# Kernel tuning notes

Measured on AMD Instinct MI355X. Metric: run time of the kernel, lower is better.

Reference implementation:

```python
import jax, jax.numpy as jnp
import numpy as np

N_LAYERS = 6
D_MODEL = 256
D_STATE_C = 32  # d_state=64 real -> 32 complex conjugate pairs
N_MELS = 128
NUM_CLASSES = 50
BATCH = 16
SEQ = 2048


def setup_inputs() -> dict:
    key = jax.random.key(0)
    ks = jax.random.split(key, 16)
    H, N, NL = D_MODEL, D_STATE_C, N_LAYERS
    dt_min, dt_max = 1e-3, 1e-1
    log_dt = (jax.random.uniform(ks[0], (NL, H)) * (np.log(dt_max) - np.log(dt_min))
              + np.log(dt_min)).astype(jnp.float32)
    # S4D-Lin style init for the diagonal state matrix (proxy for NPLR legs)
    A_re = -0.5 * jnp.ones((NL, H, N), jnp.float32)
    A_im = jnp.broadcast_to(np.pi * jnp.arange(N, dtype=jnp.float32), (NL, H, N))
    A_im = jnp.asarray(A_im)
    return {
        'x': jax.random.normal(ks[1], (BATCH, SEQ, N_MELS), jnp.float32),
        'W_in': jax.random.normal(ks[2], (N_MELS, H), jnp.float32) / np.sqrt(N_MELS),
        'b_in': jnp.zeros((H,), jnp.float32),
        'log_dt': log_dt,
        'A_re': A_re,
        'A_im': A_im,
        'B_re': jax.random.normal(ks[3], (NL, H, N), jnp.float32),
        'B_im': jax.random.normal(ks[4], (NL, H, N), jnp.float32),
        'C_re': jax.random.normal(ks[5], (NL, H, N), jnp.float32),
        'C_im': jax.random.normal(ks[6], (NL, H, N), jnp.float32),
        'D': jax.random.normal(ks[7], (NL, H), jnp.float32),
        'W_out': jax.random.normal(ks[8], (NL, H, 2 * H), jnp.float32) / np.sqrt(H),
        'b_out': jnp.zeros((NL, 2 * H), jnp.float32),
        'ln_scale': jnp.ones((NL, H), jnp.float32),
        'ln_bias': jnp.zeros((NL, H), jnp.float32),
        'ln_f_scale': jnp.ones((H,), jnp.float32),
        'ln_f_bias': jnp.zeros((H,), jnp.float32),
        'W_cls': jax.random.normal(ks[9], (H, NUM_CLASSES), jnp.float32) / np.sqrt(H),
        'b_cls': jnp.zeros((NUM_CLASSES,), jnp.float32),
    }


def _layer_norm(x, scale, bias, eps=1e-5):
    mu = jnp.mean(x, axis=-1, keepdims=True)
    var = jnp.mean(jnp.square(x - mu), axis=-1, keepdims=True)
    return (x - mu) * jax.lax.rsqrt(var + eps) * scale + bias


def _forward(x, W_in, b_in, log_dt, A_re, A_im, B_re, B_im, C_re, C_im, D,
             W_out, b_out, ln_scale, ln_bias, ln_f_scale, ln_f_bias, W_cls, b_cls):
    x = x @ W_in + b_in  # [B, L, H]
    L = x.shape[1]
    t = jnp.arange(L, dtype=jnp.float32)
    n_fft = 2 * L
    for i in range(N_LAYERS):
        z = _layer_norm(x, ln_scale[i], ln_bias[i])  # prenorm
        A = A_re[i] + 1j * A_im[i]                   # [H, N] complex diag
        Bc = B_re[i] + 1j * B_im[i]
        Cc = C_re[i] + 1j * C_im[i]
        dt = jnp.exp(log_dt[i])[:, None]             # [H, 1]
        dtA = dt * A
        dB = Bc * (jnp.exp(dtA) - 1.0) / A           # ZOH discretization
        # K[h, l] = 2 Re( sum_n C*dB * exp(l * dt * A) )  -- conjugate-pair SSM kernel
        van = jnp.exp(dtA[:, :, None] * t)            # [H, N, L]
        K = 2.0 * jnp.einsum('hn,hnl->hl', Cc * dB, van).real
        # FFT convolution along time
        u_f = jnp.fft.rfft(z, n=n_fft, axis=1)        # [B, n/2+1, H]
        k_f = jnp.fft.rfft(K, n=n_fft, axis=-1)       # [H, n/2+1]
        y = jnp.fft.irfft(u_f * k_f.T[None], n=n_fft, axis=1)[:, :L]
        y = y + z * D[i]                              # skip (D) term
        y = jax.nn.gelu(y)                            # activation
        v = y @ W_out[i] + b_out[i]                   # [B, L, 2H]
        a, g = jnp.split(v, 2, axis=-1)
        y = a * jax.nn.sigmoid(g)                     # GLU postact
        x = x + y                                     # residual 'R'
    x = _layer_norm(x, ln_f_scale, ln_f_bias)         # final prenorm norm
    pooled = jnp.mean(x, axis=1)                      # NDDecoder mode='pool'
    return pooled @ W_cls + b_cls                     # [B, num_classes]


def reference(x, W_in, b_in, log_dt, A_re, A_im, B_re, B_im, C_re, C_im, D,
              W_out, b_out, ln_scale, ln_bias, ln_f_scale, ln_f_bias, W_cls, b_cls):
    return _forward(x, W_in, b_in, log_dt, A_re, A_im, B_re, B_im, C_re, C_im, D,
                    W_out, b_out, ln_scale, ln_bias, ln_f_scale, ln_f_bias, W_cls, b_cls)
```

## Files before the change

### kernel.cpp

```cpp
#include <hip/hip_runtime.h>
#include <math.h>

#define NLAYERS 6
#define HD 256
#define NS 32
#define NCLS 50
#define BB 16
#define LL 2048
#define TT 64
#define CC 32

typedef __attribute__((ext_vector_type(8))) short bf16x8;
typedef __attribute__((ext_vector_type(4))) float f32x4;

__device__ __attribute__((aligned(16))) float g_x [8388608];
__device__ __attribute__((aligned(16))) float g_Vt[6389760];
__device__ __attribute__((aligned(16))) float g_Kt[98304];
__device__ __attribute__((aligned(16))) float g_E0[98304];
__device__ __attribute__((aligned(16))) float g_pp[65536];
__device__ __attribute__((aligned(16))) unsigned short g_zbh[8388608];
__device__ __attribute__((aligned(16))) unsigned short g_Mt [12582912];
__device__ __attribute__((aligned(16))) unsigned short g_TAt[6291456];
__device__ __attribute__((aligned(16))) unsigned short g_ybh[8388608];
__device__ __attribute__((aligned(16))) unsigned short g_yt [8388608];
__device__ __attribute__((aligned(16))) unsigned short g_Wt [786432];
__device__ __attribute__((aligned(16))) unsigned short g_xb [4194304];
__device__ __attribute__((aligned(16))) unsigned short g_Wint[32768];

__device__ __forceinline__ float sigf(float x) { return 1.0f / (1.0f + __expf(-x)); }
__device__ __forceinline__ float geluf(float x) {
  float t = 0.7978845608028654f * (x + 0.044715f * x * x * x);
  float e = __expf(2.0f * t);
  float th = 1.0f - 2.0f / (e + 1.0f);
  return 0.5f * x * (1.0f + th);
}
__device__ __forceinline__ unsigned short f2bf(float f) {
  unsigned u = __float_as_uint(f);
  unsigned r = (u + 0x7FFFu + ((u >> 16) & 1u)) >> 16;
  return (unsigned short)r;
}

__global__ void k_precomp(const float* __restrict__ log_dt,
                          const float* __restrict__ A_re, const float* __restrict__ A_im,
                          const float* __restrict__ B_re, const float* __restrict__ B_im,
                          const float* __restrict__ C_re, const float* __restrict__ C_im) {
  int id = blockIdx.x * 256 + threadIdx.x;
  if (id >= NLAYERS * HD * NS) return;
  int h = (id / NS) % HD;
  int i = id / (NS * HD);
  float dt = expf(log_dt[i * HD + h]);
  float ar = A_re[id], ai = A_im[id];
  float dr = dt * ar, di = dt * ai;
  float er = expf(dr);
  float wr = er * cosf(di), wi = er * sinf(di);
  float inv = 1.0f / (ar * ar + ai * ai);
  float mr = wr - 1.0f, mi = wi;
  float qr = (mr * ar + mi * ai) * inv;
  float qi = (mi * ar - mr * ai) * inv;
  float br = B_re[id], bi = B_im[id];
  float dbr = br * qr - bi * qi, dbi = br * qi + bi * qr;
  float cr = C_re[id], ci = C_im[id];
  g_E0[id * 2 + 0] = cr * dbr - ci * dbi;
  g_E0[id * 2 + 1] = cr * dbi + ci * dbr;
  float pr = 1.0f, pi = 0.0f;
  long base = (long)id * 65;
  for (int t = 0; t <= 64; ++t) {
    g_Vt[(base + t) * 2 + 0] = pr;
    g_Vt[(base + t) * 2 + 1] = pi;
    float nr = pr * wr - pi * wi;
    pi = pr * wi + pi * wr;
    pr = nr;
  }
}

__global__ void k_precompK() {
  int id = blockIdx.x * 256 + threadIdx.x;
  if (id >= NLAYERS * HD * TT) return;
  int t = id % TT;
  int lh = id / TT;
  float acc = 0.f;
  const float* e = g_E0 + (long)lh * NS * 2;
  const float* v = g_Vt + ((long)lh * NS * 65 + t) * 2;
  for (int n = 0; n < NS; ++n)
    acc += e[n * 2] * v[n * 130] - e[n * 2 + 1] * v[n * 130 + 1];
  g_Kt[id] = 2.0f * acc;
}

__global__ void k_precompM(const float* __restrict__ Dd) {
  int id = blockIdx.x * 256 + threadIdx.x;
  int k = id & 127;
  int t = (id >> 7) & 63;
  int lh = id >> 13;
  float v;
  if (k < 64) {
    v = (t >= k) ? g_Kt[(long)lh * 64 + (t - k)] : 0.f;
    if (k == t) v += Dd[lh];
  } else {
    int p = k - 64, n = p >> 1;
    const float2 w = ((const float2*)g_Vt)[((long)lh * NS + n) * 65 + (t + 1)];
    v = (p & 1) ? (-2.f * w.y) : (2.f * w.x);
  }
  g_Mt[id] = f2bf(v);
}

__global__ void k_precompA2() {
  int id = blockIdx.x * 256 + threadIdx.x;
  int t = id & 63;
  int p = (id >> 6) & 63;
  int lh = id >> 12;
  int n = p >> 1;
  const float2 w = ((const float2*)g_Vt)[((long)lh * NS + n) * 65 + (63 - t)];
  g_TAt[id] = f2bf((p & 1) ? w.y : w.x);
}

__global__ __launch_bounds__(256) void k_prepW(const float* __restrict__ W_out) {
  __shared__ float T[32][33];
  int bid = blockIdx.x;
  int nt = bid & 15, kt = (bid >> 4) & 7, l = bid >> 7;
  int t = threadIdx.x;
  int tr = t >> 3, tc = t & 7;
  const float* src = W_out + (long)l * 131072 + (long)(kt * 32) * 512 + nt * 32;
  float4 v = *(const float4*)(src + (long)tr * 512 + tc * 4);
  T[tr][tc * 4 + 0] = v.x; T[tr][tc * 4 + 1] = v.y;
  T[tr][tc * 4 + 2] = v.z; T[tr][tc * 4 + 3] = v.w;
  __syncthreads();
  ushort4 o;
  o.x = f2bf(T[tc * 4 + 0][tr]); o.y = f2bf(T[tc * 4 + 1][tr]);
  o.z = f2bf(T[tc * 4 + 2][tr]); o.w = f2bf(T[tc * 4 + 3][tr]);
  *(ushort4*)(g_Wt + ((long)l * 512 + nt * 32 + tr) * 256 + kt * 32 + tc * 4) = o;
}

__global__ void k_prepWin(const float* __restrict__ W_in) {
  int k = blockIdx.x, n = threadIdx.x;
  g_Wint[n * 128 + k] = f2bf(W_in[k * 256 + n]);
}

__global__ void k_castin(const float* __restrict__ xin) {
  long base = ((long)blockIdx.x * 256 + threadIdx.x) * 8;
  float4 v0 = *(const float4*)(xin + base);
  float4 v1 = *(const float4*)(xin + base + 4);
  union { unsigned short u[8]; ulonglong2 v; } pk;
  pk.u[0] = f2bf(v0.x); pk.u[1] = f2bf(v0.y); pk.u[2] = f2bf(v0.z); pk.u[3] = f2bf(v0.w);
  pk.u[4] = f2bf(v1.x); pk.u[5] = f2bf(v1.y); pk.u[6] = f2bf(v1.z); pk.u[7] = f2bf(v1.w);
  *(ulonglong2*)(g_xb + base) = pk.v;
}

__global__ __launch_bounds__(256) void k_gemmin(const float* __restrict__ bias) {
  __shared__ __attribute__((aligned(16))) unsigned short As[128 * 32];
  __shared__ __attribute__((aligned(16))) unsigned short Bs[256 * 32];
  const int tid = threadIdx.x;
  const int wave = tid >> 6, lane = tid & 63;
  const int m0 = blockIdx.x * 128;
  const int wm = wave & 1, wn = wave >> 1;
  const int n15 = lane & 15, kg = lane >> 4, q2 = kg * 8;
  f32x4 acc[4][8];
  #pragma unroll
  for (int a = 0; a < 4; ++a)
    #pragma unroll
    for (int b2 = 0; b2 < 8; ++b2) acc[a][b2] = (f32x4){0.f, 0.f, 0.f, 0.f};
  for (int k0 = 0; k0 < 128; k0 += 32) {
    __syncthreads();
    #pragma unroll
    for (int it = 0; it < 2; ++it) {
      int slot = it * 256 + wave * 64 + lane;
      int m = slot >> 2, ko = (slot & 3) * 8;
      __builtin_amdgcn_global_load_lds(
        (const __attribute__((address_space(1))) unsigned int*)(g_xb + (long)(m0 + m) * 128 + k0 + ko),
        (__attribute__((address_space(3))) unsigned int*)(As + (it * 256 + wave * 64) * 8),
        16, 0, 0);
    }
    #pragma unroll
    for (int it = 0; it < 4; ++it) {
      int slot = it * 256 + wave * 64 + lane;
      int n = slot >> 2, ko = (slot & 3) * 8;
      __builtin_amdgcn_global_load_lds(
        (const __attribute__((address_space(1))) unsigned int*)(g_Wint + (long)n * 128 + k0 + ko),
        (__attribute__((address_space(3))) unsigned int*)(Bs + (it * 256 + wave * 64) * 8),
        16, 0, 0);
    }
    __syncthreads();
    bf16x8 af[4], bn[8];
    #pragma unroll
    for (int mt = 0; mt < 4; ++mt)
      af[mt] = *(const bf16x8*)&As[(wm * 64 + mt * 16 + n15) * 32 + q2];
    #pragma unroll
    for (int j = 0; j < 8; ++j)
      bn[j] = *(const bf16x8*)&Bs[(wn * 128 + j * 16 + n15) * 32 + q2];
    #pragma unroll
    for (int mt = 0; mt < 4; ++mt)
      #pragma unroll
      for (int j = 0; j < 8; ++j)
        acc[mt][j] = __builtin_amdgcn_mfma_f32_16x16x32_bf16(af[mt], bn[j], acc[mt][j], 0, 0, 0);
  }
  #pragma unroll
  for (int j = 0; j < 8; ++j) {
    int col = wn * 128 + j * 16 + n15;
    float bb = bias[col];
    #pragma unroll
    for (int mt = 0; mt < 4; ++mt)
      #pragma unroll
      for (int r = 0; r < 4; ++r) {
        int row = m0 + wm * 64 + mt * 16 + kg * 4 + r;
        g_x[(long)row * 256 + col] = acc[mt][j][r] + bb;
      }
  }
}

__global__ __launch_bounds__(256) void k_ln(const float* __restrict__ gam,
                                            const float* __restrict__ bet) {
  __shared__ unsigned short S[32 * 264];
  const int bid = blockIdx.x;
  const int b = bid >> 6, l0 = (bid & 63) << 5;
  const int tid = threadIdx.x, w = tid >> 6, lane = tid & 63;
  float4 gv = *(const float4*)(gam + lane * 4);
  float4 bv = *(const float4*)(bet + lane * 4);
  for (int r = 0; r < 8; ++r) {
    int ll = w * 8 + r;
    float4 v = *(const float4*)(g_x + ((long)(b * LL + l0 + ll)) * HD + lane * 4);
    float s1 = v.x + v.y + v.z + v.w;
    float s2 = v.x * v.x + v.y * v.y + v.z * v.z + v.w * v.w;
    #pragma unroll
    for (int off = 32; off; off >>= 1) { s1 += __shfl_xor(s1, off); s2 += __shfl_xor(s2, off); }
    float mu = s1 * (1.0f / HD);
    float rs = rsqrtf(s2 * (1.0f / HD) - mu * mu + 1e-5f);
    ushort4 o;
    o.x = f2bf((v.x - mu) * rs * gv.x + bv.x);
    o.y = f2bf((v.y - mu) * rs * gv.y + bv.y);
    o.z = f2bf((v.z - mu) * rs * gv.z + bv.z);
    o.w = f2bf((v.w - mu) * rs * gv.w + bv.w);
    *(ushort4*)&S[ll * 264 + lane * 4] = o;
  }
  __syncthreads();
  unsigned short* zp = g_zbh + ((long)(b * HD + tid)) * LL + l0;
  #pragma unroll
  for (int seg = 0; seg < 4; ++seg) {
    union { unsigned short u[8]; ulonglong2 v; } pk;
    #pragma unroll
    for (int i = 0; i < 8; ++i) pk.u[i] = S[(seg * 8 + i) * 264 + tid];
    *(ulonglong2*)(zp + seg * 8) = pk.v;
  }
}

__global__ __launch_bounds__(256) void k_ssm(int layer) {
  __shared__ __attribute__((aligned(16))) unsigned short Zs[32 * 72];
  __shared__ __attribute__((aligned(16))) unsigned short Ts[64 * 72];
  __shared__ __attribute__((aligned(16))) unsigned short Ms[64 * 136];
  __shared__ float Ss[32 * 68];
  __shared__ __attribute__((aligned(16))) unsigned short Gs[32 * 72];
  const int tid = threadIdx.x, wave = tid >> 6, lane = tid & 63;
  const int h = blockIdx.x >> 4, b = blockIdx.x & 15;
  const long lh = (long)layer * HD + h;
  {
    int c = tid >> 3, off = (tid & 7) * 8;
    *(ulonglong2*)&Zs[c * 72 + off] =
        *(const ulonglong2*)(g_zbh + ((long)(b * HD + h)) * LL + c * 64 + off);
  }
  const unsigned short* Tg = g_TAt + lh * 4096;
  #pragma unroll
  for (int i = 0; i < 2; ++i) {
    int seg = tid + i * 256;
    int row = seg >> 3, sc = (seg & 7) * 8;
    *(ulonglong2*)&Ts[row * 72 + sc] = *(const ulonglong2*)(Tg + row * 64 + sc);
  }
  const unsigned short* Mg = g_Mt + lh * 8192;
  #pragma unroll
  for (int i = 0; i < 4; ++i) {
    int seg = tid + i * 256;
    int row = seg >> 4, sc = (seg & 15) * 8;
    *(ulonglong2*)&Ms[row * 136 + sc] = *(const ulonglong2*)(Mg + row * 128 + sc);
  }
  __syncthreads();
  const int n15 = lane & 15, kg = lane >> 4;
  const int mt = wave & 1;
  const int jb = (wave >> 1) * 2;
  const int c = mt * 16 + n15;
  {
    bf16x8 a0 = *(const bf16x8*)&Zs[c * 72 + kg * 8];
    bf16x8 a1 = *(const bf16x8*)&Zs[c * 72 + 32 + kg * 8];
    #pragma unroll
    for (int jj = 0; jj < 2; ++jj) {
      int j = jb + jj;
      bf16x8 b0 = *(const bf16x8*)&Ts[(j * 16 + n15) * 72 + kg * 8];
      bf16x8 b1 = *(const bf16x8*)&Ts[(j * 16 + n15) * 72 + 32 + kg * 8];
      f32x4 acc = (f32x4){0.f, 0.f, 0.f, 0.f};
      acc = __builtin_amdgcn_mfma_f32_16x16x32_bf16(a0, b0, acc, 0, 0, 0);
      acc = __builtin_amdgcn_mfma_f32_16x16x32_bf16(a1, b1, acc, 0, 0, 0);
      #pragma unroll
      for (int r = 0; r < 4; ++r)
        Ss[(mt * 16 + kg * 4 + r) * 68 + j * 16 + n15] = acc[r];
    }
  }
  __syncthreads();
  if (wave == 0 && lane < 32) {
    int n = lane;
    long vb = (lh * NS + n) * 65;
    float wtr = g_Vt[vb * 2 + 128], wti = g_Vt[vb * 2 + 129];
    float e0r = g_E0[(lh * NS + n) * 2], e0i = g_E0[(lh * NS + n) * 2 + 1];
    float sr = 0.f, si = 0.f;
    for (int cc = 0; cc < CC; ++cc) {
      float er = Ss[cc * 68 + 2 * n], ei = Ss[cc * 68 + 2 * n + 1];
      Gs[cc * 72 + 2 * n]     = f2bf(e0r * sr - e0i * si);
      Gs[cc * 72 + 2 * n + 1] = f2bf(e0r * si + e0i * sr);
      float nr = er + wtr * sr - wti * si;
      si      = ei + wtr * si + wti * sr;
      sr = nr;
    }
  }
  __syncthreads();
  {
    bf16x8 a0 = *(const bf16x8*)&Zs[c * 72 + kg * 8];
    bf16x8 a1 = *(const bf16x8*)&Zs[c * 72 + 32 + kg * 8];
    bf16x8 a2 = *(const bf16x8*)&Gs[c * 72 + kg * 8];
    bf16x8 a3 = *(const bf16x8*)&Gs[c * 72 + 32 + kg * 8];
    unsigned short* yrow = g_ybh + ((long)(b * HD + h)) * LL;
    #pragma unroll
    for (int jj = 0; jj < 2; ++jj) {
      int j = jb + jj;
      const unsigned short* mrow = &Ms[(j * 16 + n15) * 136];
      bf16x8 b0 = *(const bf16x8*)&mrow[kg * 8];
      bf16x8 b1 = *(const bf16x8*)&mrow[32 + kg * 8];
      bf16x8 b2 = *(const bf16x8*)&mrow[64 + kg * 8];
      bf16x8 b3 = *(const bf16x8*)&mrow[96 + kg * 8];
      f32x4 acc = (f32x4){0.f, 0.f, 0.f, 0.f};
      acc = __builtin_amdgcn_mfma_f32_16x16x32_bf16(a0, b0, acc, 0, 0, 0);
      acc = __builtin_amdgcn_mfma_f32_16x16x32_bf16(a1, b1, acc, 0, 0, 0);
      acc = __builtin_amdgcn_mfma_f32_16x16x32_bf16(a2, b2, acc, 0, 0, 0);
      acc = __builtin_amdgcn_mfma_f32_16x16x32_bf16(a3, b3, acc, 0, 0, 0);
      #pragma unroll
      for (int r = 0; r < 4; ++r)
        yrow[(mt * 16 + kg * 4 + r) * 64 + j * 16 + n15] = f2bf(geluf(acc[r]));
    }
  }
}

__global__ __launch_bounds__(256) void k_transp() {
  __shared__ unsigned short T[64][65];
  int bid = blockIdx.x;
  int ht = bid & 3, lt = (bid >> 2) & 31, b = bid >> 7;
  int t = threadIdx.x;
  int r = t >> 4, c = t & 15;
  #pragma unroll
  for (int i = 0; i < 4; ++i) {
    int hh = r + i * 16;
    ushort4 v = *(const ushort4*)(g_ybh + ((long)(b * 256 + ht * 64 + hh)) * 2048 + lt * 64 + c * 4);
    T[hh][c * 4 + 0] = v.x; T[hh][c * 4 + 1] = v.y;
    T[hh][c * 4 + 2] = v.z; T[hh][c * 4 + 3] = v.w;
  }
  __syncthreads();
  #pragma unroll
  for (int i = 0; i < 4; ++i) {
    int ll = r + i * 16;
    ushort4 o;
    o.x = T[c * 4 + 0][ll]; o.y = T[c * 4 + 1][ll];
    o.z = T[c * 4 + 2][ll]; o.w = T[c * 4 + 3][ll];
    *(ushort4*)(g_yt + ((long)(b * 2048 + lt * 64 + ll)) * 256 + ht * 64 + c * 4) = o;
  }
}

__global__ __launch_bounds__(256, 4) void k_gemmglu(int layer, const float* __restrict__ bias) {
  __shared__ __attribute__((aligned(16))) unsigned short As[64 * 32];
  __shared__ __attribute__((aligned(16))) unsigned short Bs[256 * 32];
  const int tid = threadIdx.x;
  const int wave = tid >> 6, lane = tid & 63;
  const int m0 = blockIdx.x * 64;
  const int gg = blockIdx.y;
  const int wm = wave & 1, wn = wave >> 1;
  const int n15 = lane & 15, kg = lane >> 4, q2 = kg * 8;
  const unsigned short* Ag = g_yt + (long)m0 * 256;
  const unsigned short* Wt = g_Wt + (long)layer * 131072;
  f32x4 acc[2][8];
  #pragma unroll
  for (int a = 0; a < 2; ++a)
    #pragma unroll
    for (int b2 = 0; b2 < 8; ++b2) acc[a][b2] = (f32x4){0.f, 0.f, 0.f, 0.f};
  for (int k0 = 0; k0 < 256; k0 += 32) {
    __syncthreads();
    {
      int slot = wave * 64 + lane;
      int m = slot >> 2, ko = (slot & 3) * 8;
      __builtin_amdgcn_global_load_lds(
        (const __attribute__((address_space(1))) unsigned int*)(Ag + (long)m * 256 + k0 + ko),
        (__attribute__((address_space(3))) unsigned int*)(As + (wave * 64) * 8),
        16, 0, 0);
    }
    #pragma unroll
    for (int it = 0; it < 4; ++it) {
      int slot = it * 256 + wave * 64 + lane;
      int np = slot >> 2, ko = (slot & 3) * 8;
      int n = gg * 128 + (np < 128 ? np : np + 128);
      __builtin_amdgcn_global_load_lds(
        (const __attribute__((address_space(1))) unsigned int*)(Wt + (long)n * 256 + k0 + ko),
        (__attribute__((address_space(3))) unsigned int*)(Bs + (it * 256 + wave * 64) * 8),
        16, 0, 0);
    }
    __syncthreads();
    bf16x8 af0 = *(const bf16x8*)&As[(wm * 32 + n15) * 32 + q2];
    bf16x8 af1 = *(const bf16x8*)&As[(wm * 32 + 16 + n15) * 32 + q2];
    #pragma unroll
    for (int j = 0; j < 4; ++j) {
      bf16x8 ba = *(const bf16x8*)&Bs[(wn * 64 + j * 16 + n15) * 32 + q2];
      acc[0][j] = __builtin_amdgcn_mfma_f32_16x16x32_bf16(af0, ba, acc[0][j], 0, 0, 0);
      acc[1][j] = __builtin_amdgcn_mfma_f32_16x16x32_bf16(af1, ba, acc[1][j], 0, 0, 0);
      bf16x8 bg = *(const bf16x8*)&Bs[(128 + wn * 64 + j * 16 + n15) * 32 + q2];
      acc[0][4 + j] = __builtin_amdgcn_mfma_f32_16x16x32_bf16(af0, bg, acc[0][4 + j], 0, 0, 0);
      acc[1][4 + j] = __builtin_amdgcn_mfma_f32_16x16x32_bf16(af1, bg, acc[1][4 + j], 0, 0, 0);
    }
  }
  #pragma unroll
  for (int j = 0; j < 4; ++j) {
    int col = gg * 128 + wn * 64 + j * 16 + n15;
    float ba = bias[col], bg = bias[col + 256];
    #pragma unroll
    for (int mt = 0; mt < 2; ++mt) {
      #pragma unroll
      for (int r = 0; r < 4; ++r) {
        int row = m0 + wm * 32 + mt * 16 + kg * 4 + r;
        float a = acc[mt][j][r] + ba;
        float g = acc[mt][4 + j][r] + bg;
        float* xp = g_x + (long)row * 256 + col;
        *xp += a * sigf(g);
      }
    }
  }
}

__global__ __launch_bounds__(256) void k_lnpool(const float* __restrict__ gam,
                                                const float* __restrict__ bet) {
  __shared__ float red[4][256];
  const int bid = blockIdx.x;
  const int b = bid >> 4, s = bid & 15;
  const int tid = threadIdx.x, w = tid >> 6, lane = tid & 63;
  float4 gv = *(const float4*)(gam + lane * 4);
  float4 bv = *(const float4*)(bet + lane * 4);
  float a0 = 0, a1 = 0, a2 = 0, a3 = 0;
  for (int r = 0; r < 32; ++r) {
    int l = s * 128 + w * 32 + r;
    float4 v = *(const float4*)(g_x + ((long)b * LL + l) * HD + lane * 4);
    float s1 = v.x + v.y + v.z + v.w;
    float s2 = v.x * v.x + v.y * v.y + v.z * v.z + v.w * v.w;
    #pragma unroll
    for (int off = 32; off; off >>= 1) { s1 += __shfl_xor(s1, off); s2 += __shfl_xor(s2, off); }
    float mu = s1 * (1.0f / HD);
    float rs = rsqrtf(s2 * (1.0f / HD) - mu * mu + 1e-5f);
    a0 += (v.x - mu) * rs * gv.x + bv.x;
    a1 += (v.y - mu) * rs * gv.y + bv.y;
    a2 += (v.z - mu) * rs * gv.z + bv.z;
    a3 += (v.w - mu) * rs * gv.w + bv.w;
  }
  red[w][lane * 4 + 0] = a0; red[w][lane * 4 + 1] = a1;
  red[w][lane * 4 + 2] = a2; red[w][lane * 4 + 3] = a3;
  __syncthreads();
  g_pp[(long)bid * HD + tid] = red[0][tid] + red[1][tid] + red[2][tid] + red[3][tid];
}

__global__ __launch_bounds__(256) void k_cls(const float* __restrict__ Wc,
                                             const float* __restrict__ bc,
                                             float* __restrict__ out) {
  __shared__ float pl[256];
  const int b = blockIdx.x, tid = threadIdx.x;
  float p = 0.f;
  #pragma unroll
  for (int s = 0; s < 16; ++s) p += g_pp[((long)b * 16 + s) * HD + tid];
  pl[tid] = p * (1.0f / LL);
  __syncthreads();
  if (tid < NCLS) {
    float acc = bc[tid];
    for (int h = 0; h < HD; ++h) acc += pl[h] * Wc[h * NCLS + tid];
    out[b * NCLS + tid] = acc;
  }
}

extern "C" void kernel_launch(void* const* d_in, const int* in_sizes, int n_in,
                              void* d_out, int out_size, void* d_ws, size_t ws_size,
                              hipStream_t stream) {
  (void)in_sizes; (void)n_in; (void)d_ws; (void)ws_size; (void)out_size;
  const float* x_in   = (const float*)d_in[0];
  const float* W_in   = (const float*)d_in[1];
  const float* b_in   = (const float*)d_in[2];
  const float* log_dt = (const float*)d_in[3];
  const float* A_re   = (const float*)d_in[4];
  const float* A_im   = (const float*)d_in[5];
  const float* B_re   = (const float*)d_in[6];
  const float* B_im   = (const float*)d_in[7];
  const float* C_re   = (const float*)d_in[8];
  const float* C_im   = (const float*)d_in[9];
  const float* Dd     = (const float*)d_in[10];
  const float* W_out  = (const float*)d_in[11];
  const float* b_out  = (const float*)d_in[12];
  const float* ln_s   = (const float*)d_in[13];
  const float* ln_b   = (const float*)d_in[14];
  const float* lnf_s  = (const float*)d_in[15];
  const float* lnf_b  = (const float*)d_in[16];
  const float* W_cls  = (const float*)d_in[17];
  const float* b_cl   = (const float*)d_in[18];
  float* out = (float*)d_out;

  k_precomp<<<192, 256, 0, stream>>>(log_dt, A_re, A_im, B_re, B_im, C_re, C_im);
  k_precompK<<<384, 256, 0, stream>>>();
  k_precompM<<<49152, 256, 0, stream>>>(Dd);
  k_precompA2<<<24576, 256, 0, stream>>>();
  k_prepW<<<768, 256, 0, stream>>>(W_out);
  k_prepWin<<<128, 256, 0, stream>>>(W_in);
  k_castin<<<2048, 256, 0, stream>>>(x_in);
  k_gemmin<<<256, 256, 0, stream>>>(b_in);
  for (int i = 0; i < NLAYERS; ++i) {
    k_ln<<<1024, 256, 0, stream>>>(ln_s + i * HD, ln_b + i * HD);
    k_ssm<<<4096, 256, 0, stream>>>(i);
    k_transp<<<2048, 256, 0, stream>>>();
    k_gemmglu<<<dim3(512, 2), 256, 0, stream>>>(i, b_out + i * 2 * HD);
  }
  k_lnpool<<<256, 256, 0, stream>>>(lnf_s, lnf_b);
  k_cls<<<16, 256, 0, stream>>>(W_cls, b_cl, out);
}
```

Before: 720.1 us.

## Fuse transpose and next-layer LayerNorm into GLU GEMM epilogue

Removes the separate transpose kernel by having the GLU GEMM read the SSM output in [B,H,L] layout directly and transpose it into shared memory. It also fuses the next layer's LayerNorm into the GEMM epilogue: each block now covers all 512 output columns for 32 rows, so it can compute row statistics and write normalized bf16 z in [B,H,L] layout. This cuts two kernel launches per layer and the associated global round trips of the activations. In exchange the blocks are smaller in M, the shared-memory footprint is larger, and the A-tile loads are narrow strided 8-byte reads.

After: 710.4 us. About the same (-1.3%).

```diff
diff --git a/kernel.cpp b/kernel.cpp
--- a/kernel.cpp
+++ b/kernel.cpp
@@ -22,7 +22,6 @@
 __device__ __attribute__((aligned(16))) unsigned short g_Mt [12582912];
 __device__ __attribute__((aligned(16))) unsigned short g_TAt[6291456];
 __device__ __attribute__((aligned(16))) unsigned short g_ybh[8388608];
-__device__ __attribute__((aligned(16))) unsigned short g_yt [8388608];
 __device__ __attribute__((aligned(16))) unsigned short g_Wt [786432];
 __device__ __attribute__((aligned(16))) unsigned short g_xb [4194304];
 __device__ __attribute__((aligned(16))) unsigned short g_Wint[32768];
@@ -333,41 +332,22 @@
   }
 }
 
-__global__ __launch_bounds__(256) void k_transp() {
-  __shared__ unsigned short T[64][65];
-  int bid = blockIdx.x;
-  int ht = bid & 3, lt = (bid >> 2) & 31, b = bid >> 7;
-  int t = threadIdx.x;
-  int r = t >> 4, c = t & 15;
-  #pragma unroll
-  for (int i = 0; i < 4; ++i) {
-    int hh = r + i * 16;
-    ushort4 v = *(const ushort4*)(g_ybh + ((long)(b * 256 + ht * 64 + hh)) * 2048 + lt * 64 + c * 4);
-    T[hh][c * 4 + 0] = v.x; T[hh][c * 4 + 1] = v.y;
-    T[hh][c * 4 + 2] = v.z; T[hh][c * 4 + 3] = v.w;
-  }
-  __syncthreads();
-  #pragma unroll
-  for (int i = 0; i < 4; ++i) {
-    int ll = r + i * 16;
-    ushort4 o;
-    o.x = T[c * 4 + 0][ll]; o.y = T[c * 4 + 1][ll];
-    o.z = T[c * 4 + 2][ll]; o.w = T[c * 4 + 3][ll];
-    *(ushort4*)(g_yt + ((long)(b * 2048 + lt * 64 + ll)) * 256 + ht * 64 + c * 4) = o;
-  }
-}
-
-__global__ __launch_bounds__(256, 4) void k_gemmglu(int layer, const float* __restrict__ bias) {
-  __shared__ __attribute__((aligned(16))) unsigned short As[64 * 32];
-  __shared__ __attribute__((aligned(16))) unsigned short Bs[256 * 32];
-  const int tid = threadIdx.x;
-  const int wave = tid >> 6, lane = tid & 63;
-  const int m0 = blockIdx.x * 64;
-  const int gg = blockIdx.y;
-  const int wm = wave & 1, wn = wave >> 1;
+__global__ __launch_bounds__(256, 4) void k_gemmglu(int layer, const float* __restrict__ bias,
+                                                    const float* __restrict__ gam,
+                                                    const float* __restrict__ bet,
+                                                    int writez) {
+  __shared__ __attribute__((aligned(16))) unsigned short As[32 * 40];
+  __shared__ __attribute__((aligned(16))) float UU[8448];
+  __shared__ float Rs1[32][4], Rs2[32][4], muS[32], rsS[32];
+  unsigned short* Bs = (unsigned short*)UU;
+  float* Xs = UU;
+  const int tid = threadIdx.x, wave = tid >> 6, lane = tid & 63;
   const int n15 = lane & 15, kg = lane >> 4, q2 = kg * 8;
-  const unsigned short* Ag = g_yt + (long)m0 * 256;
+  const int row0 = blockIdx.x * 32;
+  const int b = row0 >> 11, l0 = row0 & 2047;
   const unsigned short* Wt = g_Wt + (long)layer * 131072;
+  const unsigned short* ybase = g_ybh + (long)b * HD * LL + l0;
+  const int hl = tid >> 3, sg = tid & 7;
   f32x4 acc[2][8];
   #pragma unroll
   for (int a = 0; a < 2; ++a)
@@ -375,52 +355,101 @@
     for (int b2 = 0; b2 < 8; ++b2) acc[a][b2] = (f32x4){0.f, 0.f, 0.f, 0.f};
   for (int k0 = 0; k0 < 256; k0 += 32) {
     __syncthreads();
-    {
-      int slot = wave * 64 + lane;
-      int m = slot >> 2, ko = (slot & 3) * 8;
-      __builtin_amdgcn_global_load_lds(
-        (const __attribute__((address_space(1))) unsigned int*)(Ag + (long)m * 256 + k0 + ko),
-        (__attribute__((address_space(3))) unsigned int*)(As + (wave * 64) * 8),
-        16, 0, 0);
-    }
-    #pragma unroll
-    for (int it = 0; it < 4; ++it) {
+    ushort4 av = *(const ushort4*)(ybase + (long)(k0 + hl) * LL + sg * 4);
+    As[(sg * 4 + 0) * 40 + hl] = av.x;
+    As[(sg * 4 + 1) * 40 + hl] = av.y;
+    As[(sg * 4 + 2) * 40 + hl] = av.z;
+    As[(sg * 4 + 3) * 40 + hl] = av.w;
+    #pragma unroll
+    for (int it = 0; it < 8; ++it) {
       int slot = it * 256 + wave * 64 + lane;
-      int np = slot >> 2, ko = (slot & 3) * 8;
-      int n = gg * 128 + (np < 128 ? np : np + 128);
+      int n = slot >> 2, ko = (slot & 3) * 8;
       __builtin_amdgcn_global_load_lds(
         (const __attribute__((address_space(1))) unsigned int*)(Wt + (long)n * 256 + k0 + ko),
         (__attribute__((address_space(3))) unsigned int*)(Bs + (it * 256 + wave * 64) * 8),
         16, 0, 0);
     }
     __syncthreads();
-    bf16x8 af0 = *(const bf16x8*)&As[(wm * 32 + n15) * 32 + q2];
-    bf16x8 af1 = *(const bf16x8*)&As[(wm * 32 + 16 + n15) * 32 + q2];
+    bf16x8 af0 = *(const bf16x8*)&As[(n15) * 40 + q2];
+    bf16x8 af1 = *(const bf16x8*)&As[(16 + n15) * 40 + q2];
     #pragma unroll
     for (int j = 0; j < 4; ++j) {
-      bf16x8 ba = *(const bf16x8*)&Bs[(wn * 64 + j * 16 + n15) * 32 + q2];
+      int nc = wave * 64 + j * 16 + n15;
+      bf16x8 ba = *(const bf16x8*)&Bs[nc * 32 + q2];
       acc[0][j] = __builtin_amdgcn_mfma_f32_16x16x32_bf16(af0, ba, acc[0][j], 0, 0, 0);
       acc[1][j] = __builtin_amdgcn_mfma_f32_16x16x32_bf16(af1, ba, acc[1][j], 0, 0, 0);
-      bf16x8 bg = *(const bf16x8*)&Bs[(128 + wn * 64 + j * 16 + n15) * 32 + q2];
+      bf16x8 bg = *(const bf16x8*)&Bs[(nc + 256) * 32 + q2];
       acc[0][4 + j] = __builtin_amdgcn_mfma_f32_16x16x32_bf16(af0, bg, acc[0][4 + j], 0, 0, 0);
       acc[1][4 + j] = __builtin_amdgcn_mfma_f32_16x16x32_bf16(af1, bg, acc[1][4 + j], 0, 0, 0);
     }
   }
+  __syncthreads();
+  float s1l[2][4], s2l[2][4];
+  #pragma unroll
+  for (int mt = 0; mt < 2; ++mt)
+    #pragma unroll
+    for (int r = 0; r < 4; ++r) { s1l[mt][r] = 0.f; s2l[mt][r] = 0.f; }
   #pragma unroll
   for (int j = 0; j < 4; ++j) {
-    int col = gg * 128 + wn * 64 + j * 16 + n15;
+    int col = wave * 64 + j * 16 + n15;
     float ba = bias[col], bg = bias[col + 256];
     #pragma unroll
     for (int mt = 0; mt < 2; ++mt) {
       #pragma unroll
       for (int r = 0; r < 4; ++r) {
-        int row = m0 + wm * 32 + mt * 16 + kg * 4 + r;
+        int rl = mt * 16 + kg * 4 + r;
+        long xi = (long)(row0 + rl) * 256 + col;
         float a = acc[mt][j][r] + ba;
         float g = acc[mt][4 + j][r] + bg;
-        float* xp = g_x + (long)row * 256 + col;
-        *xp += a * sigf(g);
+        float xn = g_x[xi] + a * sigf(g);
+        g_x[xi] = xn;
+        if (writez) {
+          Xs[col * 33 + rl] = xn;
+          s1l[mt][r] += xn; s2l[mt][r] += xn * xn;
+        }
       }
     }
+  }
+  if (!writez) return;
+  #pragma unroll
+  for (int mt = 0; mt < 2; ++mt)
+    #pragma unroll
+    for (int r = 0; r < 4; ++r) {
+      #pragma unroll
+      for (int off = 1; off < 16; off <<= 1) {
+        s1l[mt][r] += __shfl_xor(s1l[mt][r], off);
+        s2l[mt][r] += __shfl_xor(s2l[mt][r], off);
+      }
+    }
+  if (n15 == 0) {
+    #pragma unroll
+    for (int mt = 0; mt < 2; ++mt)
+      #pragma unroll
+      for (int r = 0; r < 4; ++r) {
+        Rs1[mt * 16 + kg * 4 + r][wave] = s1l[mt][r];
+        Rs2[mt * 16 + kg * 4 + r][wave] = s2l[mt][r];
+      }
+  }
+  __syncthreads();
+  if (tid < 32) {
+    float s1 = Rs1[tid][0] + Rs1[tid][1] + Rs1[tid][2] + Rs1[tid][3];
+    float s2 = Rs2[tid][0] + Rs2[tid][1] + Rs2[tid][2] + Rs2[tid][3];
+    float mu = s1 * (1.0f / HD);
+    float rs = rsqrtf(s2 * (1.0f / HD) - mu * mu + 1e-5f);
+    muS[tid] = mu; rsS[tid] = rs;
+  }
+  __syncthreads();
+  {
+    int hh = tid;
+    float gm = gam[hh], bt = bet[hh];
+    const float* xrow = &Xs[hh * 33];
+    union { unsigned short u[32]; ulonglong2 v4[4]; } pk;
+    #pragma unroll
+    for (int rl = 0; rl < 32; ++rl)
+      pk.u[rl] = f2bf((xrow[rl] - muS[rl]) * rsS[rl] * gm + bt);
+    unsigned short* zp = g_zbh + ((long)(b * HD + hh)) * LL + l0;
+    #pragma unroll
+    for (int q = 0; q < 4; ++q) *(ulonglong2*)(zp + q * 8) = pk.v4[q];
   }
 }
 
@@ -503,11 +532,13 @@
   k_prepWin<<<128, 256, 0, stream>>>(W_in);
   k_castin<<<2048, 256, 0, stream>>>(x_in);
   k_gemmin<<<256, 256, 0, stream>>>(b_in);
+  k_ln<<<1024, 256, 0, stream>>>(ln_s, ln_b);
   for (int i = 0; i < NLAYERS; ++i) {
-    k_ln<<<1024, 256, 0, stream>>>(ln_s + i * HD, ln_b + i * HD);
+    int nl = (i + 1 < NLAYERS) ? (i + 1) : 0;
     k_ssm<<<4096, 256, 0, stream>>>(i);
-    k_transp<<<2048, 256, 0, stream>>>();
-    k_gemmglu<<<dim3(512, 2), 256, 0, stream>>>(i, b_out + i * 2 * HD);
+    k_gemmglu<<<1024, 256, 0, stream>>>(i, b_out + i * 2 * HD,
+                                        ln_s + nl * HD, ln_b + nl * HD,
+                                        (i + 1 < NLAYERS) ? 1 : 0);
   }
   k_lnpool<<<256, 256, 0, stream>>>(lnf_s, lnf_b);
   k_cls<<<16, 256, 0, stream>>>(W_cls, b_cl, out);
```
